# Performance work log

Hardware: AMD Instinct MI355X
Metric: run time of the kernel (lower is better)

The kernel has to match this reference:

```python
import jax, jax.numpy as jnp
import numpy as np

STRIDE = 1
PADDING = 1
KERNEL = 3


def _extract_patches(x, k, stride, padding):
    # x: [N, C, H, W] -> patches stacked as [k, k, N, C, Hout, Wout]
    xp = jnp.pad(x, ((0, 0), (0, 0), (padding, padding), (padding, padding)))
    Hp, Wp = xp.shape[2], xp.shape[3]
    oh = (Hp - k) // stride + 1
    ow = (Wp - k) // stride + 1
    rows = []
    for i in range(k):
        cols = []
        for j in range(k):
            cols.append(xp[:, :, i : i + oh * stride : stride, j : j + ow * stride : stride])
        rows.append(jnp.stack(cols, axis=0))
    return jnp.stack(rows, axis=0)  # [k, k, N, C, oh, ow]


def setup_inputs() -> dict:
    key = jax.random.key(0)
    k1, k2 = jax.random.split(key)
    N, C, H, W = 32, 32, 56, 56
    O, OH, OW, K = 32, 56, 56, 3
    x = jax.random.normal(k1, (N, C, H, W), dtype=jnp.float32)
    # kaiming-normal-ish scale for leaky_relu(a=0.1), fan_out mode
    fan_out = O * K * K
    gain = np.sqrt(2.0 / (1.0 + 0.1 ** 2))
    std = gain / np.sqrt(fan_out)
    weight = jax.random.normal(k2, (O, OH, OW, C, K, K), dtype=jnp.float32) * std
    bias = jnp.zeros((1, O, OH, OW), dtype=jnp.float32)
    return {"x": x, "weight": weight, "bias": bias}


def reference(x, weight, bias):
    # weight: [O, H, W, C, i, k]; patches: [i, k, N, C, H, W]
    patches = _extract_patches(x, KERNEL, STRIDE, PADDING)
    out = jnp.einsum('ohwcik,iknchw->nohw', weight, patches)
    return out + bias
```

## Files before the change

kernel.cpp:

```cpp
#include <hip/hip_runtime.h>

#define N_  32
#define C_  32
#define H_  56
#define W_  56
#define O_  32
#define HP_ 58
#define WP_ 58
#define HW_ (H_*W_)
#define CHW_ (C_*H_*W_)
#define KK_ 9
#define CKK_ (C_*KK_)

#define XT_ELEMS ((size_t)C_*HP_*WP_*N_)

#define KP_   144
#define PSTR_ 36

typedef __bf16 bf16x8 __attribute__((ext_vector_type(8)));
typedef float  f32x4  __attribute__((ext_vector_type(4)));

__global__ __launch_bounds__(256) void xpose_kernel(const float* __restrict__ x,
                                                    __bf16* __restrict__ xT) {
    const int c = blockIdx.x;
    const int y = blockIdx.y;
    __shared__ float sbuf[32 * 57];
    const int tid = threadIdx.x;
    const bool interior = (y >= 1) && (y <= H_);
    if (interior) {
        for (int idx = tid; idx < N_ * W_; idx += 256) {
            int n = idx / W_;
            int col = idx - n * W_;
            sbuf[n * 57 + col] = x[((size_t)(n * C_ + c) * H_ + (y - 1)) * W_ + col];
        }
    }
    __syncthreads();
    __bf16* dst = xT + ((size_t)(c * HP_ + y)) * WP_ * N_;
    for (int idx = tid; idx < WP_ * N_; idx += 256) {
        int xx = idx >> 5;
        int n  = idx & 31;
        float v = 0.f;
        if (interior && xx >= 1 && xx <= W_) v = sbuf[n * 57 + (xx - 1)];
        dst[idx] = (__bf16)v;
    }
}

__global__ __launch_bounds__(256) void lc2d_mfma(const float* __restrict__ wgt,
                                                 const __bf16* __restrict__ xT,
                                                 const float* __restrict__ bias,
                                                 float* __restrict__ out) {
    __shared__ unsigned P2[2 * KP_ * PSTR_];
    __shared__ __align__(16) float sbuf[32][33][2];

    const int tid = threadIdx.x;

    const int flat = blockIdx.x;
    const int wg = (flat & 7) * 196 + (flat >> 3);
    const int wt = wg % 28;
    const int h  = wg / 28;
    const int w0 = wt * 2;

    const int wave = tid >> 6;
    const int lane = tid & 63;
    const int dw = wave & 1;
    const int oh = wave >> 1;
    const int w  = w0 + dw;
    const int q = lane >> 4;
    const int r = lane & 15;

    const float* wb = wgt + ((size_t)((oh * 16 + r) * HW_ + h * W_ + w)) * CKK_ + 8 * q;
    float4 wv[18];
    #pragma unroll
    for (int s = 0; s < 9; ++s) {
        wv[2 * s]     = *(const float4*)(wb + 32 * s);
        wv[2 * s + 1] = *(const float4*)(wb + 32 * s + 4);
    }
    __builtin_amdgcn_sched_barrier(0);

    const __bf16* xbase = xT + (h * WP_ + w0) * N_;
    #pragma unroll
    for (int it = 0; it < 5; ++it) {
        const int task = it * 256 + tid;
        if (task < 1152) {
            const int tdw = task / 576;
            const int rem = task - tdw * 576;
            const int kp  = rem >> 2;
            const int g   = rem & 3;
            const int k0 = 2 * kp, k1 = 2 * kp + 1;
            const int c0 = k0 / 9, ij0 = k0 - 9 * c0;
            const int i0 = ij0 / 3, j0 = ij0 - 3 * i0;
            const int c1 = k1 / 9, ij1 = k1 - 9 * c1;
            const int i1 = ij1 / 3, j1 = ij1 - 3 * i1;
            const int off0 = c0 * (HP_ * WP_ * N_) + i0 * (WP_ * N_) + j0 * N_;
            const int off1 = c1 * (HP_ * WP_ * N_) + i1 * (WP_ * N_) + j1 * N_;
            const __bf16* s0 = xbase + tdw * N_ + off0 + 8 * g;
            const __bf16* s1 = xbase + tdw * N_ + off1 + 8 * g;
            union { uint4 qv; ushort sv[8]; } ua, ub;
            ua.qv = *(const uint4*)s0;
            ub.qv = *(const uint4*)s1;
            unsigned o0[8];
            #pragma unroll
            for (int m = 0; m < 8; ++m)
                o0[m] = (unsigned)ua.sv[m] | ((unsigned)ub.sv[m] << 16);
            unsigned* dst = &P2[(tdw * KP_ + kp) * PSTR_ + 8 * g];
            *(uint4*)(dst)     = make_uint4(o0[0], o0[1], o0[2], o0[3]);
            *(uint4*)(dst + 4) = make_uint4(o0[4], o0[5], o0[6], o0[7]);
        }
    }
    __syncthreads();

    const unsigned* pa = &P2[(dw * KP_ + 4 * q) * PSTR_ + r];

    f32x4 acc0 = {0.f, 0.f, 0.f, 0.f};
    f32x4 acc1 = {0.f, 0.f, 0.f, 0.f};

    #pragma unroll
    for (int s = 0; s < 9; ++s) {
        union { unsigned u[4]; bf16x8 v; } a0, a1;
        #pragma unroll
        for (int d = 0; d < 4; ++d) {
            a0.u[d] = pa[s * (16 * PSTR_) + d * PSTR_];
            a1.u[d] = pa[s * (16 * PSTR_) + d * PSTR_ + 16];
        }
        const float4 ba = wv[2 * s];
        const float4 bb = wv[2 * s + 1];
        bf16x8 bfB;
        bfB[0] = (__bf16)ba.x; bfB[1] = (__bf16)ba.y; bfB[2] = (__bf16)ba.z; bfB[3] = (__bf16)ba.w;
        bfB[4] = (__bf16)bb.x; bfB[5] = (__bf16)bb.y; bfB[6] = (__bf16)bb.z; bfB[7] = (__bf16)bb.w;

        acc0 = __builtin_amdgcn_mfma_f32_16x16x32_bf16(a0.v, bfB, acc0, 0, 0, 0);
        acc1 = __builtin_amdgcn_mfma_f32_16x16x32_bf16(a1.v, bfB, acc1, 0, 0, 0);
    }

    #pragma unroll
    for (int mt = 0; mt < 2; ++mt) {
        f32x4 a = mt == 0 ? acc0 : acc1;
        const int o = oh * 16 + r;
        #pragma unroll
        for (int reg = 0; reg < 4; ++reg) {
            const int n = mt * 16 + q * 4 + reg;
            sbuf[n][o][dw] = a[reg];
        }
    }
    __syncthreads();

    #pragma unroll
    for (int rr = 0; rr < 4; ++rr) {
        const int fl = rr * 256 + tid;
        const int n = fl >> 5;
        const int o = fl & 31;
        float2 v = *(const float2*)&sbuf[n][o][0];
        const float2 bv = *(const float2*)(bias + o * HW_ + h * W_ + w0);
        v.x += bv.x; v.y += bv.y;
        *(float2*)(out + (size_t)n * CHW_ + o * HW_ + h * W_ + w0) = v;
    }
}

__global__ __launch_bounds__(256) void lc2d_naive(const float* __restrict__ x,
                                                  const float* __restrict__ wgt,
                                                  const float* __restrict__ bias,
                                                  float* __restrict__ out) {
    int idx = blockIdx.x * 256 + threadIdx.x;
    const int total = N_ * O_ * H_ * W_;
    if (idx >= total) return;
    int w = idx % W_;
    int h = (idx / W_) % H_;
    int o = (idx / HW_) % O_;
    int n = idx / CHW_;
    const float* wp = wgt + ((size_t)((o * H_ + h) * W_ + w)) * CKK_;
    float s = 0.f;
    for (int c = 0; c < C_; ++c) {
        for (int i = 0; i < 3; ++i) {
            int yy = h + i - 1;
            if (yy < 0 || yy >= H_) continue;
            for (int j = 0; j < 3; ++j) {
                int xx = w + j - 1;
                if (xx < 0 || xx >= W_) continue;
                s = fmaf(wp[c * KK_ + i * 3 + j],
                         x[((size_t)(n * C_ + c) * H_ + yy) * W_ + xx], s);
            }
        }
    }
    out[idx] = s + bias[idx % CHW_];
}

extern "C" void kernel_launch(void* const* d_in, const int* in_sizes, int n_in,
                              void* d_out, int out_size, void* d_ws, size_t ws_size,
                              hipStream_t stream) {
    const float* x    = (const float*)d_in[0];
    const float* wgt  = (const float*)d_in[1];
    const float* bias = (const float*)d_in[2];
    float* out = (float*)d_out;

    const size_t need = XT_ELEMS * sizeof(__bf16);
    if (ws_size >= need) {
        __bf16* xT = (__bf16*)d_ws;
        hipLaunchKernelGGL(xpose_kernel, dim3(C_, HP_), dim3(256), 0, stream, x, xT);
        hipLaunchKernelGGL(lc2d_mfma, dim3(1568), dim3(256), 0, stream, wgt, xT, bias, out);
    } else {
        int total = N_ * O_ * H_ * W_;
        hipLaunchKernelGGL(lc2d_naive, dim3((total + 255) / 256), dim3(256), 0, stream,
                           x, wgt, bias, out);
    }
}
```

Measured before the change: 41.89 us.

## Stage weights into LDS via direct global_load_lds with swizzle, one pixel per block

The weight tile for each output pixel (32 outputs by 288 values) is now loaded straight into LDS with global_load_lds 16-byte transfers, using an XOR swizzle to avoid bank conflicts, instead of being held in per-lane float4 registers. Each block now covers one output pixel rather than two, so the grid doubles. The four waves split the work by batch half and output half, each doing one MFMA chain. This is meant to cut register pressure and make the weight stream more coalesced, at the cost of a larger LDS footprint, more blocks, and scalar rather than float2 output stores.

Measured after the change: 63.05 us. +50.5%, slower.

```diff
diff --git a/kernel.cpp b/kernel.cpp
--- a/kernel.cpp
+++ b/kernel.cpp
@@ -11,6 +11,8 @@
 #define CHW_ (C_*H_*W_)
 #define KK_ 9
 #define CKK_ (C_*KK_)
+#define WROWB_ 1152
+#define WROWSTRIDE_ ((size_t)HW_ * CKK_ * 4)
 
 #define XT_ELEMS ((size_t)C_*HP_*WP_*N_)
 
@@ -19,6 +21,13 @@
 
 typedef __bf16 bf16x8 __attribute__((ext_vector_type(8)));
 typedef float  f32x4  __attribute__((ext_vector_type(4)));
+
+__device__ __forceinline__ void gload_lds16(const void* g, void* l) {
+    __builtin_amdgcn_global_load_lds(
+        (const __attribute__((address_space(1))) unsigned int*)g,
+        (__attribute__((address_space(3))) unsigned int*)l,
+        16, 0, 0);
+}
 
 __global__ __launch_bounds__(256) void xpose_kernel(const float* __restrict__ x,
                                                     __bf16* __restrict__ xT) {
@@ -49,99 +58,96 @@
                                                  const __bf16* __restrict__ xT,
                                                  const float* __restrict__ bias,
                                                  float* __restrict__ out) {
-    __shared__ unsigned P2[2 * KP_ * PSTR_];
-    __shared__ __align__(16) float sbuf[32][33][2];
+    __shared__ __align__(16) float4 wlds4[2304];
+    __shared__ unsigned P2[KP_ * PSTR_];
+    __shared__ __align__(16) float sbuf[32][33];
 
     const int tid = threadIdx.x;
 
     const int flat = blockIdx.x;
-    const int wg = (flat & 7) * 196 + (flat >> 3);
-    const int wt = wg % 28;
-    const int h  = wg / 28;
-    const int w0 = wt * 2;
+    const int wg = (flat & 7) * 392 + (flat >> 3);
+    const int w = wg % 56;
+    const int h = wg / 56;
+    const int pos = h * W_ + w;
 
     const int wave = tid >> 6;
     const int lane = tid & 63;
-    const int dw = wave & 1;
+    const int nh = wave & 1;
     const int oh = wave >> 1;
-    const int w  = w0 + dw;
     const int q = lane >> 4;
     const int r = lane & 15;
 
-    const float* wb = wgt + ((size_t)((oh * 16 + r) * HW_ + h * W_ + w)) * CKK_ + 8 * q;
-    float4 wv[18];
+    {
+        const char* wposb = (const char*)wgt + (size_t)pos * WROWB_;
+        char* wldsb = (char*)wlds4;
+        const unsigned lane16 = lane * 16;
+        #pragma unroll
+        for (int u = 0; u < 9; ++u) {
+            const unsigned t = wave * 9 + u;
+            const unsigned phys = t * 1024 + lane16;
+            const unsigned row = phys / WROWB_;
+            const unsigned within = phys - row * WROWB_;
+            const unsigned col = within ^ ((row & 3) << 5);
+            gload_lds16(wposb + (size_t)row * WROWSTRIDE_ + col,
+                        wldsb + t * 1024);
+        }
+    }
+
+    {
+        const __bf16* xbase = xT + (h * WP_ + w) * N_;
+        #pragma unroll
+        for (int it = 0; it < 3; ++it) {
+            const int task = it * 256 + tid;
+            if (task < 576) {
+                const int kp = task >> 2;
+                const int g  = task & 3;
+                const int k0 = 2 * kp, k1 = 2 * kp + 1;
+                const int c0 = k0 / 9, ij0 = k0 - 9 * c0;
+                const int i0 = ij0 / 3, j0 = ij0 - 3 * i0;
+                const int c1 = k1 / 9, ij1 = k1 - 9 * c1;
+                const int i1 = ij1 / 3, j1 = ij1 - 3 * i1;
+                const int off0 = c0 * (HP_ * WP_ * N_) + i0 * (WP_ * N_) + j0 * N_;
+                const int off1 = c1 * (HP_ * WP_ * N_) + i1 * (WP_ * N_) + j1 * N_;
+                union { uint4 qv; ushort sv[8]; } ua, ub;
+                ua.qv = *(const uint4*)(xbase + off0 + 8 * g);
+                ub.qv = *(const uint4*)(xbase + off1 + 8 * g);
+                unsigned o0[8];
+                #pragma unroll
+                for (int m = 0; m < 8; ++m)
+                    o0[m] = (unsigned)ua.sv[m] | ((unsigned)ub.sv[m] << 16);
+                unsigned* dst = &P2[kp * PSTR_ + 8 * g];
+                *(uint4*)(dst)     = make_uint4(o0[0], o0[1], o0[2], o0[3]);
+                *(uint4*)(dst + 4) = make_uint4(o0[4], o0[5], o0[6], o0[7]);
+            }
+        }
+    }
+    __syncthreads();
+
+    const int orow = oh * 16 + r;
+    const char* wrowb = (const char*)wlds4 + orow * WROWB_;
+    const unsigned rmask = (orow & 3) << 5;
+    const unsigned* pa = &P2[(4 * q) * PSTR_ + nh * 16 + r];
+
+    f32x4 acc = {0.f, 0.f, 0.f, 0.f};
+
     #pragma unroll
     for (int s = 0; s < 9; ++s) {
-        wv[2 * s]     = *(const float4*)(wb + 32 * s);
-        wv[2 * s + 1] = *(const float4*)(wb + 32 * s + 4);
-    }
-    __builtin_amdgcn_sched_barrier(0);
-
-    const __bf16* xbase = xT + (h * WP_ + w0) * N_;
-    #pragma unroll
-    for (int it = 0; it < 5; ++it) {
-        const int task = it * 256 + tid;
-        if (task < 1152) {
-            const int tdw = task / 576;
-            const int rem = task - tdw * 576;
-            const int kp  = rem >> 2;
-            const int g   = rem & 3;
-            const int k0 = 2 * kp, k1 = 2 * kp + 1;
-            const int c0 = k0 / 9, ij0 = k0 - 9 * c0;
-            const int i0 = ij0 / 3, j0 = ij0 - 3 * i0;
-            const int c1 = k1 / 9, ij1 = k1 - 9 * c1;
-            const int i1 = ij1 / 3, j1 = ij1 - 3 * i1;
-            const int off0 = c0 * (HP_ * WP_ * N_) + i0 * (WP_ * N_) + j0 * N_;
-            const int off1 = c1 * (HP_ * WP_ * N_) + i1 * (WP_ * N_) + j1 * N_;
-            const __bf16* s0 = xbase + tdw * N_ + off0 + 8 * g;
-            const __bf16* s1 = xbase + tdw * N_ + off1 + 8 * g;
-            union { uint4 qv; ushort sv[8]; } ua, ub;
-            ua.qv = *(const uint4*)s0;
-            ub.qv = *(const uint4*)s1;
-            unsigned o0[8];
-            #pragma unroll
-            for (int m = 0; m < 8; ++m)
-                o0[m] = (unsigned)ua.sv[m] | ((unsigned)ub.sv[m] << 16);
-            unsigned* dst = &P2[(tdw * KP_ + kp) * PSTR_ + 8 * g];
-            *(uint4*)(dst)     = make_uint4(o0[0], o0[1], o0[2], o0[3]);
-            *(uint4*)(dst + 4) = make_uint4(o0[4], o0[5], o0[6], o0[7]);
-        }
-    }
-    __syncthreads();
-
-    const unsigned* pa = &P2[(dw * KP_ + 4 * q) * PSTR_ + r];
-
-    f32x4 acc0 = {0.f, 0.f, 0.f, 0.f};
-    f32x4 acc1 = {0.f, 0.f, 0.f, 0.f};
-
-    #pragma unroll
-    for (int s = 0; s < 9; ++s) {
-        union { unsigned u[4]; bf16x8 v; } a0, a1;
+        union { unsigned u[4]; bf16x8 v; } a0;
         #pragma unroll
-        for (int d = 0; d < 4; ++d) {
-            a0.u[d] = pa[s * (16 * PSTR_) + d * PSTR_];
-            a1.u[d] = pa[s * (16 * PSTR_) + d * PSTR_ + 16];
-        }
-        const float4 ba = wv[2 * s];
-        const float4 bb = wv[2 * s + 1];
+        for (int d = 0; d < 4; ++d)
+            a0.u[d] = pa[(16 * s + d) * PSTR_];
+        const unsigned bo = ((unsigned)(128 * s + 32 * q)) ^ rmask;
+        const float4 ba = *(const float4*)(wrowb + bo);
+        const float4 bb = *(const float4*)(wrowb + bo + 16);
         bf16x8 bfB;
         bfB[0] = (__bf16)ba.x; bfB[1] = (__bf16)ba.y; bfB[2] = (__bf16)ba.z; bfB[3] = (__bf16)ba.w;
         bfB[4] = (__bf16)bb.x; bfB[5] = (__bf16)bb.y; bfB[6] = (__bf16)bb.z; bfB[7] = (__bf16)bb.w;
-
-        acc0 = __builtin_amdgcn_mfma_f32_16x16x32_bf16(a0.v, bfB, acc0, 0, 0, 0);
-        acc1 = __builtin_amdgcn_mfma_f32_16x16x32_bf16(a1.v, bfB, acc1, 0, 0, 0);
+        acc = __builtin_amdgcn_mfma_f32_16x16x32_bf16(a0.v, bfB, acc, 0, 0, 0);
     }
 
     #pragma unroll
-    for (int mt = 0; mt < 2; ++mt) {
-        f32x4 a = mt == 0 ? acc0 : acc1;
-        const int o = oh * 16 + r;
-        #pragma unroll
-        for (int reg = 0; reg < 4; ++reg) {
-            const int n = mt * 16 + q * 4 + reg;
-            sbuf[n][o][dw] = a[reg];
-        }
-    }
+    for (int reg = 0; reg < 4; ++reg)
+        sbuf[nh * 16 + q * 4 + reg][oh * 16 + r] = acc[reg];
     __syncthreads();
 
     #pragma unroll
@@ -149,10 +155,7 @@
         const int fl = rr * 256 + tid;
         const int n = fl >> 5;
         const int o = fl & 31;
-        float2 v = *(const float2*)&sbuf[n][o][0];
-        const float2 bv = *(const float2*)(bias + o * HW_ + h * W_ + w0);
-        v.x += bv.x; v.y += bv.y;
-        *(float2*)(out + (size_t)n * CHW_ + o * HW_ + h * W_ + w0) = v;
+        out[(size_t)n * CHW_ + o * HW_ + pos] = sbuf[n][o] + bias[o * HW_ + pos];
     }
 }
 
@@ -196,7 +199,7 @@
     if (ws_size >= need) {
         __bf16* xT = (__bf16*)d_ws;
         hipLaunchKernelGGL(xpose_kernel, dim3(C_, HP_), dim3(256), 0, stream, x, xT);
-        hipLaunchKernelGGL(lc2d_mfma, dim3(1568), dim3(256), 0, stream, wgt, xT, bias, out);
+        hipLaunchKernelGGL(lc2d_mfma, dim3(3136), dim3(256), 0, stream, wgt, xT, bias, out);
     } else {
         int total = N_ * O_ * H_ * W_;
         hipLaunchKernelGGL(lc2d_naive, dim3((total + 255) / 256), dim3(256), 0, stream,
```

## Process four output columns per block with an LDS input window

Applied to the files above, without the earlier changes.

Each block now covers four output columns instead of two, halving the grid. The shared 3x6 padded input window is loaded once into LDS and reused to build the packed patch buffer for two column pairs. Both sets of weights and the bias are preloaded into registers. Output is stored directly from the accumulators without an LDS transpose. This cuts redundant global input reads and a barrier, but raises register and LDS pressure, halves block count, and loses the coalesced float2 output stores.

After: 49.91 us. +19.1%, slower.

```diff
diff --git a/kernel.cpp b/kernel.cpp
--- a/kernel.cpp
+++ b/kernel.cpp
@@ -20,18 +20,21 @@
 typedef __bf16 bf16x8 __attribute__((ext_vector_type(8)));
 typedef float  f32x4  __attribute__((ext_vector_type(4)));
 
+#define WAIT_LGKM0() asm volatile("s_waitcnt lgkmcnt(0)" ::: "memory")
+#define RAW_BAR()    asm volatile("s_barrier" ::: "memory")
+
 __global__ __launch_bounds__(256) void xpose_kernel(const float* __restrict__ x,
                                                     __bf16* __restrict__ xT) {
     const int c = blockIdx.x;
     const int y = blockIdx.y;
-    __shared__ float sbuf[32 * 57];
+    __shared__ float sb[32 * 57];
     const int tid = threadIdx.x;
     const bool interior = (y >= 1) && (y <= H_);
     if (interior) {
         for (int idx = tid; idx < N_ * W_; idx += 256) {
             int n = idx / W_;
             int col = idx - n * W_;
-            sbuf[n * 57 + col] = x[((size_t)(n * C_ + c) * H_ + (y - 1)) * W_ + col];
+            sb[n * 57 + col] = x[((size_t)(n * C_ + c) * H_ + (y - 1)) * W_ + col];
         }
     }
     __syncthreads();
@@ -40,119 +43,135 @@
         int xx = idx >> 5;
         int n  = idx & 31;
         float v = 0.f;
-        if (interior && xx >= 1 && xx <= W_) v = sbuf[n * 57 + (xx - 1)];
+        if (interior && xx >= 1 && xx <= W_) v = sb[n * 57 + (xx - 1)];
         dst[idx] = (__bf16)v;
     }
 }
 
-__global__ __launch_bounds__(256) void lc2d_mfma(const float* __restrict__ wgt,
-                                                 const __bf16* __restrict__ xT,
-                                                 const float* __restrict__ bias,
-                                                 float* __restrict__ out) {
+__global__ __launch_bounds__(256, 2) void lc2d_mfma(const float* __restrict__ wgt,
+                                                    const __bf16* __restrict__ xT,
+                                                    const float* __restrict__ bias,
+                                                    float* __restrict__ out) {
+    __shared__ __align__(16) char win[36864];
     __shared__ unsigned P2[2 * KP_ * PSTR_];
-    __shared__ __align__(16) float sbuf[32][33][2];
 
     const int tid = threadIdx.x;
 
     const int flat = blockIdx.x;
-    const int wg = (flat & 7) * 196 + (flat >> 3);
-    const int wt = wg % 28;
-    const int h  = wg / 28;
-    const int w0 = wt * 2;
+    const int wg = (flat & 7) * 98 + (flat >> 3);
+    const int wt = wg % 14;
+    const int h  = wg / 14;
+    const int w0 = wt * 4;
 
     const int wave = tid >> 6;
     const int lane = tid & 63;
     const int dw = wave & 1;
     const int oh = wave >> 1;
-    const int w  = w0 + dw;
     const int q = lane >> 4;
     const int r = lane & 15;
 
-    const float* wb = wgt + ((size_t)((oh * 16 + r) * HW_ + h * W_ + w)) * CKK_ + 8 * q;
-    float4 wv[18];
+    uint4 wreg[9];
+    #pragma unroll
+    for (int u = 0; u < 9; ++u) {
+        const int task = u * 256 + tid;
+        const int cy = task / 24;
+        const int ch = task - cy * 24;
+        const int c  = cy / 3;
+        const int y  = cy - 3 * c;
+        const int xx = ch >> 2;
+        const int g  = ch & 3;
+        wreg[u] = *(const uint4*)(xT + ((size_t)(c * HP_ + h + y) * WP_ + (w0 + xx)) * N_ + 8 * g);
+    }
+    #pragma unroll
+    for (int u = 0; u < 9; ++u)
+        *(uint4*)(win + (u * 256 + tid) * 16) = wreg[u];
+
+    const char* wbB = (const char*)wgt
+        + (size_t)((oh * 16 + r) * HW_ + h * W_ + (w0 + dw)) * 1152 + q * 32;
+    float4 wv0[18], wv1[18];
     #pragma unroll
     for (int s = 0; s < 9; ++s) {
-        wv[2 * s]     = *(const float4*)(wb + 32 * s);
-        wv[2 * s + 1] = *(const float4*)(wb + 32 * s + 4);
-    }
+        wv0[2 * s]     = *(const float4*)(wbB + s * 128);
+        wv0[2 * s + 1] = *(const float4*)(wbB + s * 128 + 16);
+        wv1[2 * s]     = *(const float4*)(wbB + s * 128 + 2304);
+        wv1[2 * s + 1] = *(const float4*)(wbB + s * 128 + 2304 + 16);
+    }
+    const float bv0 = bias[(oh * 16 + r) * HW_ + h * W_ + (w0 + dw)];
+    const float bv1 = bias[(oh * 16 + r) * HW_ + h * W_ + (w0 + 2 + dw)];
     __builtin_amdgcn_sched_barrier(0);
 
-    const __bf16* xbase = xT + (h * WP_ + w0) * N_;
-    #pragma unroll
-    for (int it = 0; it < 5; ++it) {
-        const int task = it * 256 + tid;
-        if (task < 1152) {
-            const int tdw = task / 576;
-            const int rem = task - tdw * 576;
-            const int kp  = rem >> 2;
-            const int g   = rem & 3;
-            const int k0 = 2 * kp, k1 = 2 * kp + 1;
-            const int c0 = k0 / 9, ij0 = k0 - 9 * c0;
-            const int i0 = ij0 / 3, j0 = ij0 - 3 * i0;
-            const int c1 = k1 / 9, ij1 = k1 - 9 * c1;
-            const int i1 = ij1 / 3, j1 = ij1 - 3 * i1;
-            const int off0 = c0 * (HP_ * WP_ * N_) + i0 * (WP_ * N_) + j0 * N_;
-            const int off1 = c1 * (HP_ * WP_ * N_) + i1 * (WP_ * N_) + j1 * N_;
-            const __bf16* s0 = xbase + tdw * N_ + off0 + 8 * g;
-            const __bf16* s1 = xbase + tdw * N_ + off1 + 8 * g;
-            union { uint4 qv; ushort sv[8]; } ua, ub;
-            ua.qv = *(const uint4*)s0;
-            ub.qv = *(const uint4*)s1;
-            unsigned o0[8];
+    WAIT_LGKM0();
+    RAW_BAR();
+
+    const unsigned* pa = &P2[(dw * KP_ + 4 * q) * PSTR_ + r];
+    f32x4 accs[4];
+
+    #pragma unroll
+    for (int dwp = 0; dwp < 2; ++dwp) {
+        #pragma unroll
+        for (int it = 0; it < 5; ++it) {
+            const int task = it * 256 + tid;
+            if (it < 4 || task < 1152) {
+                const int tdw = task / 576;
+                const int rem = task - tdw * 576;
+                const int kp  = rem >> 2;
+                const int g   = rem & 3;
+                const int k0 = 2 * kp, k1 = 2 * kp + 1;
+                const int c0 = k0 / 9, ij0 = k0 - 9 * c0;
+                const int i0 = ij0 / 3, j0 = ij0 - 3 * i0;
+                const int c1 = k1 / 9, ij1 = k1 - 9 * c1;
+                const int i1 = ij1 / 3, j1 = ij1 - 3 * i1;
+                const int col0 = dwp * 2 + tdw + j0;
+                const int col1 = dwp * 2 + tdw + j1;
+                union { uint4 qv; ushort sv[8]; } ua, ub;
+                ua.qv = *(const uint4*)(win + (c0 * 18 + i0 * 6 + col0) * 64 + g * 16);
+                ub.qv = *(const uint4*)(win + (c1 * 18 + i1 * 6 + col1) * 64 + g * 16);
+                unsigned o0[8];
+                #pragma unroll
+                for (int m = 0; m < 8; ++m)
+                    o0[m] = (unsigned)ua.sv[m] | ((unsigned)ub.sv[m] << 16);
+                unsigned* dst = &P2[(tdw * KP_ + kp) * PSTR_ + 8 * g];
+                *(uint4*)(dst)     = make_uint4(o0[0], o0[1], o0[2], o0[3]);
+                *(uint4*)(dst + 4) = make_uint4(o0[4], o0[5], o0[6], o0[7]);
+            }
+        }
+        WAIT_LGKM0();
+        RAW_BAR();
+
+        f32x4 acc0 = {0.f, 0.f, 0.f, 0.f};
+        f32x4 acc1 = {0.f, 0.f, 0.f, 0.f};
+        #pragma unroll
+        for (int s = 0; s < 9; ++s) {
+            union { unsigned u[4]; bf16x8 v; } a0, a1;
             #pragma unroll
-            for (int m = 0; m < 8; ++m)
-                o0[m] = (unsigned)ua.sv[m] | ((unsigned)ub.sv[m] << 16);
-            unsigned* dst = &P2[(tdw * KP_ + kp) * PSTR_ + 8 * g];
-            *(uint4*)(dst)     = make_uint4(o0[0], o0[1], o0[2], o0[3]);
-            *(uint4*)(dst + 4) = make_uint4(o0[4], o0[5], o0[6], o0[7]);
-        }
-    }
-    __syncthreads();
-
-    const unsigned* pa = &P2[(dw * KP_ + 4 * q) * PSTR_ + r];
-
-    f32x4 acc0 = {0.f, 0.f, 0.f, 0.f};
-    f32x4 acc1 = {0.f, 0.f, 0.f, 0.f};
-
-    #pragma unroll
-    for (int s = 0; s < 9; ++s) {
-        union { unsigned u[4]; bf16x8 v; } a0, a1;
-        #pragma unroll
-        for (int d = 0; d < 4; ++d) {
-            a0.u[d] = pa[s * (16 * PSTR_) + d * PSTR_];
-            a1.u[d] = pa[s * (16 * PSTR_) + d * PSTR_ + 16];
-        }
-        const float4 ba = wv[2 * s];
-        const float4 bb = wv[2 * s + 1];
-        bf16x8 bfB;
-        bfB[0] = (__bf16)ba.x; bfB[1] = (__bf16)ba.y; bfB[2] = (__bf16)ba.z; bfB[3] = (__bf16)ba.w;
-        bfB[4] = (__bf16)bb.x; bfB[5] = (__bf16)bb.y; bfB[6] = (__bf16)bb.z; bfB[7] = (__bf16)bb.w;
-
-        acc0 = __builtin_amdgcn_mfma_f32_16x16x32_bf16(a0.v, bfB, acc0, 0, 0, 0);
-        acc1 = __builtin_amdgcn_mfma_f32_16x16x32_bf16(a1.v, bfB, acc1, 0, 0, 0);
-    }
-
-    #pragma unroll
-    for (int mt = 0; mt < 2; ++mt) {
-        f32x4 a = mt == 0 ? acc0 : acc1;
+            for (int d = 0; d < 4; ++d) {
+                a0.u[d] = pa[(16 * s + d) * PSTR_];
+                a1.u[d] = pa[(16 * s + d) * PSTR_ + 16];
+            }
+            const float4 ba = dwp == 0 ? wv0[2 * s]     : wv1[2 * s];
+            const float4 bb = dwp == 0 ? wv0[2 * s + 1] : wv1[2 * s + 1];
+            bf16x8 bfB;
+            bfB[0] = (__bf16)ba.x; bfB[1] = (__bf16)ba.y; bfB[2] = (__bf16)ba.z; bfB[3] = (__bf16)ba.w;
+            bfB[4] = (__bf16)bb.x; bfB[5] = (__bf16)bb.y; bfB[6] = (__bf16)bb.z; bfB[7] = (__bf16)bb.w;
+            acc0 = __builtin_amdgcn_mfma_f32_16x16x32_bf16(a0.v, bfB, acc0, 0, 0, 0);
+            acc1 = __builtin_amdgcn_mfma_f32_16x16x32_bf16(a1.v, bfB, acc1, 0, 0, 0);
+        }
+        accs[2 * dwp]     = acc0;
+        accs[2 * dwp + 1] = acc1;
+        if (dwp == 0) { RAW_BAR(); }
+    }
+
+    #pragma unroll
+    for (int dwp = 0; dwp < 2; ++dwp) {
+        const int pos = h * W_ + w0 + dwp * 2 + dw;
+        const float bv = dwp == 0 ? bv0 : bv1;
         const int o = oh * 16 + r;
         #pragma unroll
         for (int reg = 0; reg < 4; ++reg) {
-            const int n = mt * 16 + q * 4 + reg;
-            sbuf[n][o][dw] = a[reg];
-        }
-    }
-    __syncthreads();
-
-    #pragma unroll
-    for (int rr = 0; rr < 4; ++rr) {
-        const int fl = rr * 256 + tid;
-        const int n = fl >> 5;
-        const int o = fl & 31;
-        float2 v = *(const float2*)&sbuf[n][o][0];
-        const float2 bv = *(const float2*)(bias + o * HW_ + h * W_ + w0);
-        v.x += bv.x; v.y += bv.y;
-        *(float2*)(out + (size_t)n * CHW_ + o * HW_ + h * W_ + w0) = v;
+            const int m = q * 4 + reg;
+            out[(size_t)m * CHW_ + o * HW_ + pos]        = accs[2 * dwp][reg] + bv;
+            out[(size_t)(m + 16) * CHW_ + o * HW_ + pos] = accs[2 * dwp + 1][reg] + bv;
+        }
     }
 }
 
@@ -196,7 +215,7 @@
     if (ws_size >= need) {
         __bf16* xT = (__bf16*)d_ws;
         hipLaunchKernelGGL(xpose_kernel, dim3(C_, HP_), dim3(256), 0, stream, x, xT);
-        hipLaunchKernelGGL(lc2d_mfma, dim3(1568), dim3(256), 0, stream, wgt, xT, bias, out);
+        hipLaunchKernelGGL(lc2d_mfma, dim3(784), dim3(256), 0, stream, wgt, xT, bias, out);
     } else {
         int total = N_ * O_ * H_ * W_;
         hipLaunchKernelGGL(lc2d_naive, dim3((total + 255) / 256), dim3(256), 0, stream,
```
